# Performance work log

Hardware: AMD Instinct MI355X
Metric: run time of the kernel (lower is better)

The kernel has to match this reference:

```python
import jax, jax.numpy as jnp
import numpy as np

B, S = 2, 2048
IN, CD = 512, 128
HID, HEADS, DH = 1024, 8, 128
FFN, LAT, L = 4096, 256, 2


def _ln(x, s, b, eps=1e-5):
    m = x.mean(-1, keepdims=True)
    v = x.var(-1, keepdims=True)
    return (x - m) / jnp.sqrt(v + eps) * s + b


def _decay_mask():
    # D[h, n, m] = gamma_h^(n-m) for n >= m else 0; gamma_h = 1 - 2^(-5-h)
    n = jnp.arange(S)
    d = (n[:, None] - n[None, :]).astype(jnp.float32)
    mask = d >= 0
    expo = jnp.where(mask, d, 0.0)
    gammas = 1.0 - 2.0 ** (-5.0 - jnp.arange(HEADS, dtype=jnp.float32))
    return (gammas[:, None, None] ** expo[None]) * mask[None]


def setup_inputs() -> dict:
    key = jax.random.key(0)
    ks = jax.random.split(key, 20)
    f32 = jnp.float32
    def nrm(k, shape, s=0.02):
        return jax.random.normal(k, shape, f32) * s
    return {
        "x": jax.random.normal(ks[0], (B, S, IN), f32),
        "c": jax.random.normal(ks[1], (B, S, CD), f32),
        "W_in": nrm(ks[2], (IN + CD, HID)), "b_in": jnp.zeros((HID,), f32),
        "ln1_s": jnp.ones((L, HID), f32), "ln1_b": jnp.zeros((L, HID), f32),
        "Wq": nrm(ks[3], (L, HID, HID)), "Wk": nrm(ks[4], (L, HID, HID)),
        "Wv": nrm(ks[5], (L, HID, HID)), "Wg": nrm(ks[6], (L, HID, HID)),
        "Wo": nrm(ks[7], (L, HID, HID)),
        "gn_s": jnp.ones((L, HID), f32), "gn_b": jnp.zeros((L, HID), f32),
        "ln2_s": jnp.ones((L, HID), f32), "ln2_b": jnp.zeros((L, HID), f32),
        "W1": nrm(ks[8], (L, HID, FFN)), "b1": jnp.zeros((L, FFN), f32),
        "W2": nrm(ks[9], (L, FFN, HID)), "b2": jnp.zeros((L, HID), f32),
        "lnf_s": jnp.ones((HID,), f32), "lnf_b": jnp.zeros((HID,), f32),
        "W_mu": nrm(ks[10], (HID, LAT)), "b_mu": jnp.zeros((LAT,), f32),
        "W_lv": nrm(ks[11], (HID, LAT)), "b_lv": jnp.zeros((LAT,), f32),
    }


def reference(x, c, W_in, b_in, ln1_s, ln1_b, Wq, Wk, Wv, Wg, Wo, gn_s, gn_b,
              ln2_s, ln2_b, W1, b1, W2, b2, lnf_s, lnf_b, W_mu, b_mu, W_lv, b_lv):
    D = _decay_mask()                        # [H, S, S]
    h = jnp.concatenate([x, c], -1) @ W_in + b_in  # [B, S, HID]
    scale = 1.0 / np.sqrt(DH).astype(np.float32)
    for l in range(L):
        # --- multi-scale retention (parallel form) ---
        xn = _ln(h, ln1_s[l], ln1_b[l])
        q = (xn @ Wq[l]).reshape(B, S, HEADS, DH)
        k = (xn @ Wk[l]).reshape(B, S, HEADS, DH)
        v = (xn @ Wv[l]).reshape(B, S, HEADS, DH)
        scores = jnp.einsum('bnhd,bmhd->bhnm', q, k) * scale
        scores = scores * D[None]            # causal decay weighting
        o = jnp.einsum('bhnm,bmhd->bnhd', scores, v)
        # per-head group norm
        mu_ = o.mean(-1, keepdims=True)
        var_ = o.var(-1, keepdims=True)
        o = (o - mu_) / jnp.sqrt(var_ + 1e-5)
        o = o * gn_s[l].reshape(HEADS, DH) + gn_b[l].reshape(HEADS, DH)
        o = o.reshape(B, S, HID)
        g = jax.nn.silu(xn @ Wg[l])
        h = h + (g * o) @ Wo[l]
        # --- FFN ---
        xn2 = _ln(h, ln2_s[l], ln2_b[l])
        h = h + jax.nn.gelu(xn2 @ W1[l] + b1[l]) @ W2[l] + b2[l]
    h = _ln(h, lnf_s, lnf_b)
    mu = h @ W_mu + b_mu
    raw_logvar = h @ W_lv + b_lv
    std = jax.nn.softplus(0.5 * raw_logvar) + 0.001
    return mu, std
```

## Files before the change

kernel.cpp:

```cpp
#include <hip/hip_runtime.h>
#include <cmath>

typedef __bf16 bf16_t;
typedef __bf16 bf16x8 __attribute__((ext_vector_type(8)));
typedef float f32x4 __attribute__((ext_vector_type(4)));
typedef unsigned int u32x4 __attribute__((ext_vector_type(4)));

namespace {

constexpr int kS = 2048;
constexpr int kTok = 4096;
constexpr int kHid = 1024;
constexpr int kDh = 128;
constexpr float kScale = 0.08838834764831843f;

enum {
  EPI_BF16 = 0,
  EPI_BIAS_F32 = 2,
  EPI_RESID_F32 = 3,
  EPI_BIAS_GELU_BF16 = 4,
  EPI_MULV = 7,
  EPI_PART = 8,
};

__device__ __forceinline__ void gload16(const void* g, void* l) {
  __builtin_amdgcn_global_load_lds(
      (const __attribute__((address_space(1))) void*)g,
      (__attribute__((address_space(3))) void*)l, 16, 0, 0);
}

__device__ __forceinline__ f32x4 mfma16(bf16x8 a, bf16x8 b, f32x4 c) {
  return __builtin_amdgcn_mfma_f32_16x16x32_bf16(a, b, c, 0, 0, 0);
}

__device__ __forceinline__ unsigned xcd_swz(unsigned bid, unsigned nwg) {
  if ((nwg & 7u) != 0u) return bid;
  return (bid & 7u) * (nwg >> 3) + (bid >> 3);
}

__global__ __launch_bounds__(256) void build_a0_kernel(
    const float* __restrict__ x, const float* __restrict__ c,
    bf16_t* __restrict__ a0)
{
  int i = blockIdx.x * 256 + threadIdx.x;
  if (i >= kTok * 640) return;
  int t = i / 640;
  int col = i - t * 640;
  float v = (col < 512) ? x[(size_t)t * 512 + col]
                        : c[(size_t)t * 128 + (col - 512)];
  a0[i] = (bf16_t)v;
}

__global__ __launch_bounds__(256) void transpose_cast_kernel(
    const float* __restrict__ src, bf16_t* __restrict__ dst, int K, int N)
{
  __shared__ float tile[32][33];
  int n0 = blockIdx.x * 32, k0 = blockIdx.y * 32;
  int tx = threadIdx.x, ty = threadIdx.y;
#pragma unroll
  for (int ii = 0; ii < 4; ++ii) {
    int r = ty + ii * 8;
    tile[r][tx] = src[(size_t)(k0 + r) * N + (n0 + tx)];
  }
  __syncthreads();
#pragma unroll
  for (int ii = 0; ii < 4; ++ii) {
    int r = ty + ii * 8;
    dst[(size_t)(n0 + r) * K + (k0 + tx)] = (bf16_t)tile[tx][r];
  }
}

__global__ __launch_bounds__(256) void head_transpose_kernel(
    const bf16_t* __restrict__ in, int ld, bf16_t* __restrict__ out)
{
  __shared__ bf16_t tile[32][33];
  int s0 = blockIdx.x * 32;
  int d0 = blockIdx.y * 32;
  int bh = blockIdx.z;
  int b = bh >> 3, h = bh & 7;
  int tx = threadIdx.x & 31, ty = threadIdx.x >> 5;
#pragma unroll
  for (int ii = 0; ii < 4; ++ii) {
    int r = ty + ii * 8;
    tile[r][tx] = in[(size_t)(b * kS + s0 + r) * ld + h * kDh + d0 + tx];
  }
  __syncthreads();
#pragma unroll
  for (int ii = 0; ii < 4; ++ii) {
    int r = ty + ii * 8;
    out[((size_t)bh * kDh + d0 + r) * kS + s0 + tx] = tile[tx][r];
  }
}

__global__ __launch_bounds__(256) void ln_kernel(
    const float* __restrict__ H, const float* __restrict__ s,
    const float* __restrict__ b, bf16_t* __restrict__ out)
{
  const int t = blockIdx.x;
  const int tid = threadIdx.x;
  const float* row = H + (size_t)t * kHid;
  f32x4 x = *(const f32x4*)(row + tid * 4);
  float sum = x[0] + x[1] + x[2] + x[3];
  float ssq = x[0]*x[0] + x[1]*x[1] + x[2]*x[2] + x[3]*x[3];
#pragma unroll
  for (int m = 32; m >= 1; m >>= 1) {
    sum += __shfl_xor(sum, m, 64);
    ssq += __shfl_xor(ssq, m, 64);
  }
  __shared__ float red[8];
  int wave = tid >> 6;
  if ((tid & 63) == 0) { red[wave] = sum; red[4 + wave] = ssq; }
  __syncthreads();
  sum = red[0] + red[1] + red[2] + red[3];
  ssq = red[4] + red[5] + red[6] + red[7];
  float mean = sum * (1.0f / kHid);
  float var = ssq * (1.0f / kHid) - mean * mean;
  float rstd = rsqrtf(var + 1e-5f);
  bf16_t* orow = out + (size_t)t * kHid;
#pragma unroll
  for (int j = 0; j < 4; ++j) {
    int col = tid * 4 + j;
    orow[col] = (bf16_t)((x[j] - mean) * rstd * s[col] + b[col]);
  }
}

__global__ __launch_bounds__(256) void gn_gate_kernel(
    const float* __restrict__ o, const float* __restrict__ gns,
    const float* __restrict__ gnb, bf16_t* __restrict__ g, int ldg)
{
  int idx = blockIdx.x * 4 + (threadIdx.x >> 6);
  int lane = threadIdx.x & 63;
  size_t off = (size_t)idx * kDh;
  float v0 = o[off + lane * 2];
  float v1 = o[off + lane * 2 + 1];
  float sum = v0 + v1, ssq = v0 * v0 + v1 * v1;
#pragma unroll
  for (int m = 32; m >= 1; m >>= 1) {
    sum += __shfl_xor(sum, m, 64);
    ssq += __shfl_xor(ssq, m, 64);
  }
  float mean = sum * (1.0f / kDh);
  float var = ssq * (1.0f / kDh) - mean * mean;
  float rstd = rsqrtf(var + 1e-5f);
  int t = idx >> 3, h = idx & 7;
  int c0 = h * kDh + lane * 2;
  float s0 = gns[c0], s1 = gns[c0 + 1], b0 = gnb[c0], b1 = gnb[c0 + 1];
  size_t goff = (size_t)t * ldg + h * kDh + lane * 2;
  float g0 = (float)g[goff], g1 = (float)g[goff + 1];
  g0 = g0 / (1.0f + __expf(-g0));
  g1 = g1 / (1.0f + __expf(-g1));
  g[goff]     = (bf16_t)(((v0 - mean) * rstd * s0 + b0) * g0);
  g[goff + 1] = (bf16_t)(((v1 - mean) * rstd * s1 + b1) * g1);
}

template <int TM, int EPI>
__global__ __launch_bounds__(256) void gemm_kernel(
    const bf16_t* __restrict__ A, int lda, const bf16_t* __restrict__ Bt, int ldb,
    void* __restrict__ Cv, int ldc, const float* __restrict__ bias,
    const float* __restrict__ bias2, const float* __restrict__ resid,
    int M, int N, int kSpan)
{
  constexpr int MR = TM / 32;
  constexpr int ASEG = TM / 8;
  constexpr int TOT = ASEG + 16;
  constexpr int PER_WAVE = TOT / 4;
  __shared__ bf16_t As[2][TM * 64];
  __shared__ bf16_t Bs[2][128 * 64];
  const int tid = threadIdx.x;
  const int lane = tid & 63;
  const int wave = tid >> 6;
  const int wr = (wave >> 1) * (MR * 16);
  const int wc = (wave & 1) * 64;
  const unsigned nwg = gridDim.x * gridDim.y;
  const unsigned bid = xcd_swz(blockIdx.y * gridDim.x + blockIdx.x, nwg);
  const int bm = (bid % gridDim.x) * TM;
  const int bn = (bid / gridDim.x) * 128;
  const int kb = blockIdx.z * kSpan;
  const int r_ld = lane >> 3;
  const int cg = ((lane & 7) ^ r_ld) * 8;

  f32x4 acc[MR][4] = {};

  auto stage = [&](int bufi, int t) {
    int k0 = kb + t * 64;
#pragma unroll
    for (int i = 0; i < PER_WAVE; ++i) {
      int seg = wave * PER_WAVE + i;
      if (seg < ASEG) {
        int r = seg * 8 + r_ld;
        gload16(&A[(size_t)(bm + r) * lda + k0 + cg], &As[bufi][seg * 512]);
      } else {
        int s2 = seg - ASEG;
        int r = s2 * 8 + r_ld;
        gload16(&Bt[(size_t)(bn + r) * ldb + k0 + cg], &Bs[bufi][s2 * 512]);
      }
    }
  };
  auto compute = [&](int bufi) {
#pragma unroll
    for (int kk = 0; kk < 64; kk += 32) {
      const int cg0 = (kk >> 3) + (lane >> 4);
      bf16x8 af[MR], bfr[4];
#pragma unroll
      for (int m = 0; m < MR; ++m) {
        int row = wr + m * 16 + (lane & 15);
        af[m] = *(const bf16x8*)&As[bufi][row * 64 + ((cg0 ^ (row & 7)) << 3)];
      }
#pragma unroll
      for (int n = 0; n < 4; ++n) {
        int row = wc + n * 16 + (lane & 15);
        bfr[n] = *(const bf16x8*)&Bs[bufi][row * 64 + ((cg0 ^ (row & 7)) << 3)];
      }
#pragma unroll
      for (int m = 0; m < MR; ++m)
#pragma unroll
        for (int n = 0; n < 4; ++n)
          acc[m][n] = mfma16(af[m], bfr[n], acc[m][n]);
    }
  };

  const int nt = kSpan >> 6;
  stage(0, 0);
  stage(1, 1);
  for (int t = 0; t < nt; ++t) {
    if (t + 1 < nt) {
      if constexpr (PER_WAVE == 8) asm volatile("s_waitcnt vmcnt(8)" ::: "memory");
      else                         asm volatile("s_waitcnt vmcnt(6)" ::: "memory");
    } else {
      asm volatile("s_waitcnt vmcnt(0)" ::: "memory");
    }
    __builtin_amdgcn_s_barrier();
    compute(t & 1);
    __builtin_amdgcn_s_barrier();
    if (t + 2 < nt) stage(t & 1, t + 2);
  }

  const int cr = (lane >> 4) * 4;
  const int cc = lane & 15;
#pragma unroll
  for (int m = 0; m < MR; ++m) {
#pragma unroll
    for (int n = 0; n < 4; ++n) {
#pragma unroll
      for (int j = 0; j < 4; ++j) {
        int gr = bm + wr + m * 16 + cr + j;
        int gc = bn + wc + n * 16 + cc;
        size_t off = (size_t)gr * ldc + gc;
        float v = acc[m][n][j];
        if constexpr (EPI == EPI_BF16) {
          ((bf16_t*)Cv)[off] = (bf16_t)v;
        } else if constexpr (EPI == EPI_BIAS_F32) {
          ((float*)Cv)[off] = v + bias[gc];
        } else if constexpr (EPI == EPI_RESID_F32) {
          ((float*)Cv)[off] = v + resid[off];
        } else if constexpr (EPI == EPI_BIAS_GELU_BF16) {
          v += bias[gc];
          float u3 = v + 0.044715f * v * v * v;
          float th = tanhf(0.7978845608028654f * u3);
          ((bf16_t*)Cv)[off] = (bf16_t)(0.5f * v * (1.0f + th));
        } else if constexpr (EPI == EPI_PART) {
          ((float*)Cv)[(size_t)blockIdx.z * M * N + off] = v;
        } else if constexpr (EPI == EPI_MULV) {
          if (gc < 256) {
            ((float*)Cv)[(size_t)gr * 256 + gc] = v + bias[gc];
          } else {
            float r2 = 0.5f * (v + bias2[gc - 256]);
            float sp = (r2 > 20.0f) ? r2 : log1pf(__expf(r2));
            ((float*)Cv)[(size_t)4096 * 256 + (size_t)gr * 256 + (gc - 256)] = sp + 0.001f;
          }
        }
      }
    }
  }
}

template <int EPI>
__global__ __launch_bounds__(512, 2) void gemm256_kernel(
    const bf16_t* __restrict__ A, int lda, const bf16_t* __restrict__ Bt, int ldb,
    void* __restrict__ Cv, int ldc, const float* __restrict__ bias,
    int M, int N, int kSpan)
{
  __shared__ bf16_t As[2][256 * 64];
  __shared__ bf16_t Bs[2][256 * 64];
  const int tid = threadIdx.x;
  const int lane = tid & 63;
  const int wave = tid >> 6;
  const int wm = wave >> 2;
  const int wn = wave & 3;
  const unsigned nwg = gridDim.x * gridDim.y;
  const unsigned bid = xcd_swz(blockIdx.y * gridDim.x + blockIdx.x, nwg);
  const int bm = (bid % gridDim.x) * 256;
  const int bn = (bid / gridDim.x) * 256;
  const int kb = blockIdx.z * kSpan;
  const int r_ld = lane >> 3;
  const int cgs = ((lane & 7) ^ r_ld) * 8;
  const int rl15 = lane & 15, rl7 = lane & 7, rhi = lane >> 4;

  f32x4 acc[8][4] = {};

  const bf16_t* pA0a; const bf16_t* pA0b;
  const bf16_t* pA1a; const bf16_t* pA1b;
  const bf16_t* pB0a; const bf16_t* pB0b;
  const bf16_t* pB1a; const bf16_t* pB1b;
  int sg0a, sg0b, sg1a, sg1b;
  {
    int s0a = 0 * 16 + wave * 2 + 0, s0b = 0 * 16 + wave * 2 + 1;
    int s1a = 1 * 16 + wave * 2 + 0, s1b = 1 * 16 + wave * 2 + 1;
    sg0a = s0a * 512; sg0b = s0b * 512; sg1a = s1a * 512; sg1b = s1b * 512;
    pA0a = A + (size_t)(bm + s0a * 8 + r_ld) * lda + kb + cgs;
    pA0b = A + (size_t)(bm + s0b * 8 + r_ld) * lda + kb + cgs;
    pA1a = A + (size_t)(bm + s1a * 8 + r_ld) * lda + kb + cgs;
    pA1b = A + (size_t)(bm + s1b * 8 + r_ld) * lda + kb + cgs;
    pB0a = Bt + (size_t)(bn + s0a * 8 + r_ld) * ldb + kb + cgs;
    pB0b = Bt + (size_t)(bn + s0b * 8 + r_ld) * ldb + kb + cgs;
    pB1a = Bt + (size_t)(bn + s1a * 8 + r_ld) * ldb + kb + cgs;
    pB1b = Bt + (size_t)(bn + s1b * 8 + r_ld) * ldb + kb + cgs;
  }
  auto stageA0 = [&](int bufi) {
    gload16(pA0a, &As[bufi][sg0a]); gload16(pA0b, &As[bufi][sg0b]);
  };
  auto stageA1 = [&](int bufi) {
    gload16(pA1a, &As[bufi][sg1a]); gload16(pA1b, &As[bufi][sg1b]);
  };
  auto stageB0 = [&](int bufi) {
    gload16(pB0a, &Bs[bufi][sg0a]); gload16(pB0b, &Bs[bufi][sg0b]);
  };
  auto stageB1 = [&](int bufi) {
    gload16(pB1a, &Bs[bufi][sg1a]); gload16(pB1b, &Bs[bufi][sg1b]);
  };
  auto advance = [&]() {
    pA0a += 64; pA0b += 64; pA1a += 64; pA1b += 64;
    pB0a += 64; pB0b += 64; pB1a += 64; pB1b += 64;
  };
  auto lda_frag = [&](int bufi, int mf, int kk) -> bf16x8 {
    int row = wm * 128 + mf * 16 + rl15;
    int cg0 = (kk >> 3) + rhi;
    return *(const bf16x8*)&As[bufi][row * 64 + ((cg0 ^ rl7) << 3)];
  };
  auto ldb_frag = [&](int bufi, int nf, int kk) -> bf16x8 {
    int row = wn * 64 + nf * 16 + rl15;
    int cg0 = (kk >> 3) + rhi;
    return *(const bf16x8*)&Bs[bufi][row * 64 + ((cg0 ^ rl7) << 3)];
  };

  const int nt = kSpan >> 6;
  stageA0(0); stageB0(0); stageB1(0); stageA1(0);
  advance();

  bf16x8 bk0[4], bk1[4], af[4];
  int cb = 0;

  for (int t = 0; t < nt - 1; ++t) {
    const int nb = cb ^ 1;
    asm volatile("s_waitcnt vmcnt(4)" ::: "memory");
    __builtin_amdgcn_s_barrier();
#pragma unroll
    for (int nf = 0; nf < 4; ++nf) bk0[nf] = ldb_frag(cb, nf, 0);
#pragma unroll
    for (int mf = 0; mf < 4; ++mf) af[mf] = lda_frag(cb, mf, 0);
    stageA0(nb); stageB0(nb);
    asm volatile("s_waitcnt lgkmcnt(0)" ::: "memory");
    __builtin_amdgcn_sched_barrier(0);
    __builtin_amdgcn_s_setprio(1);
#pragma unroll
    for (int mf = 0; mf < 4; ++mf)
#pragma unroll
      for (int nf = 0; nf < 4; ++nf)
        acc[mf][nf] = mfma16(af[mf], bk0[nf], acc[mf][nf]);
    __builtin_amdgcn_s_setprio(0);
    asm volatile("s_waitcnt vmcnt(6)" ::: "memory");
    __builtin_amdgcn_s_barrier();
#pragma unroll
    for (int nf = 0; nf < 4; ++nf) bk1[nf] = ldb_frag(cb, nf, 32);
#pragma unroll
    for (int mf = 0; mf < 4; ++mf) af[mf] = lda_frag(cb, mf, 32);
    stageB1(nb);
    asm volatile("s_waitcnt lgkmcnt(0)" ::: "memory");
    __builtin_amdgcn_sched_barrier(0);
    __builtin_amdgcn_s_setprio(1);
#pragma unroll
    for (int mf = 0; mf < 4; ++mf)
#pragma unroll
      for (int nf = 0; nf < 4; ++nf)
        acc[mf][nf] = mfma16(af[mf], bk1[nf], acc[mf][nf]);
    __builtin_amdgcn_s_setprio(0);
    asm volatile("s_waitcnt vmcnt(6)" ::: "memory");
    __builtin_amdgcn_s_barrier();
#pragma unroll
    for (int mf = 0; mf < 4; ++mf) af[mf] = lda_frag(cb, 4 + mf, 0);
    stageA1(nb);
    asm volatile("s_waitcnt lgkmcnt(0)" ::: "memory");
    __builtin_amdgcn_sched_barrier(0);
    __builtin_amdgcn_s_setprio(1);
#pragma unroll
    for (int mf = 0; mf < 4; ++mf)
#pragma unroll
      for (int nf = 0; nf < 4; ++nf)
        acc[4 + mf][nf] = mfma16(af[mf], bk0[nf], acc[4 + mf][nf]);
    __builtin_amdgcn_s_setprio(0);
#pragma unroll
    for (int mf = 0; mf < 4; ++mf) af[mf] = lda_frag(cb, 4 + mf, 32);
    asm volatile("s_waitcnt lgkmcnt(0)" ::: "memory");
    __builtin_amdgcn_sched_barrier(0);
    __builtin_amdgcn_s_setprio(1);
#pragma unroll
    for (int mf = 0; mf < 4; ++mf)
#pragma unroll
      for (int nf = 0; nf < 4; ++nf)
        acc[4 + mf][nf] = mfma16(af[mf], bk1[nf], acc[4 + mf][nf]);
    __builtin_amdgcn_s_setprio(0);
    advance();
    cb ^= 1;
  }

  {
    asm volatile("s_waitcnt vmcnt(0)" ::: "memory");
    __builtin_amdgcn_s_barrier();
#pragma unroll
    for (int nf = 0; nf < 4; ++nf) bk0[nf] = ldb_frag(cb, nf, 0);
#pragma unroll
    for (int nf = 0; nf < 4; ++nf) bk1[nf] = ldb_frag(cb, nf, 32);
#pragma unroll
    for (int half = 0; half < 2; ++half) {
#pragma unroll
      for (int mf = 0; mf < 4; ++mf) af[mf] = lda_frag(cb, half * 4 + mf, 0);
      asm volatile("s_waitcnt lgkmcnt(0)" ::: "memory");
      __builtin_amdgcn_sched_barrier(0);
#pragma unroll
      for (int mf = 0; mf < 4; ++mf)
#pragma unroll
        for (int nf = 0; nf < 4; ++nf)
          acc[half * 4 + mf][nf] = mfma16(af[mf], bk0[nf], acc[half * 4 + mf][nf]);
#pragma unroll
      for (int mf = 0; mf < 4; ++mf) af[mf] = lda_frag(cb, half * 4 + mf, 32);
      asm volatile("s_waitcnt lgkmcnt(0)" ::: "memory");
      __builtin_amdgcn_sched_barrier(0);
#pragma unroll
      for (int mf = 0; mf < 4; ++mf)
#pragma unroll
        for (int nf = 0; nf < 4; ++nf)
          acc[half * 4 + mf][nf] = mfma16(af[mf], bk1[nf], acc[half * 4 + mf][nf]);
    }
  }

  const int cr = rhi * 4;
  const int cc = rl15;
#pragma unroll
  for (int mf = 0; mf < 8; ++mf) {
#pragma unroll
    for (int nf = 0; nf < 4; ++nf) {
#pragma unroll
      for (int j = 0; j < 4; ++j) {
        int gr = bm + wm * 128 + mf * 16 + cr + j;
        int gc = bn + wn * 64 + nf * 16 + cc;
        size_t off = (size_t)gr * ldc + gc;
        float v = acc[mf][nf][j];
        if constexpr (EPI == EPI_BF16) {
          ((bf16_t*)Cv)[off] = (bf16_t)v;
        } else if constexpr (EPI == EPI_BIAS_GELU_BF16) {
          v += bias[gc];
          float u3 = v + 0.044715f * v * v * v;
          float th = tanhf(0.7978845608028654f * u3);
          ((bf16_t*)Cv)[off] = (bf16_t)(0.5f * v * (1.0f + th));
        } else if constexpr (EPI == EPI_PART) {
          ((float*)Cv)[(size_t)blockIdx.z * M * N + off] = v;
        }
      }
    }
  }
}

__global__ __launch_bounds__(256) void ffn2_reduce_kernel(
    const float* __restrict__ P, const float* __restrict__ b2,
    float* __restrict__ H)
{
  int i = blockIdx.x * 256 + threadIdx.x;
  size_t e = (size_t)i * 4;
  int col = (int)(e & 1023);
  f32x4 a = *(const f32x4*)&P[e];
  f32x4 b = *(const f32x4*)&P[(size_t)4096 * 1024 + e];
  f32x4 h = *(const f32x4*)&H[e];
  f32x4 bb = *(const f32x4*)&b2[col];
  f32x4 r = { h[0] + a[0] + b[0] + bb[0], h[1] + a[1] + b[1] + bb[1],
              h[2] + a[2] + b[2] + bb[2], h[3] + a[3] + b[3] + bb[3] };
  *(f32x4*)&H[e] = r;
}

__global__ __launch_bounds__(256) void chunk_state_kernel(
    const bf16_t* __restrict__ KT, const bf16_t* __restrict__ VT,
    bf16_t* __restrict__ U)
{
  __shared__ bf16_t Ka[128][72];
  __shared__ bf16_t Va[128][72];
  const int tid = threadIdx.x, lane = tid & 63, wave = tid >> 6;
  const int t = blockIdx.x, bh = blockIdx.y, h = bh & 7;
  const float lg2g = log2f(1.0f - exp2f(-5.0f - (float)h));
#pragma unroll
  for (int it = 0; it < 4; ++it) {
    int u = tid + it * 256;
    int r = u >> 3, cg = (u & 7) * 8;
    size_t g = ((size_t)bh * kDh + r) * kS + t * 64 + cg;
    *(u32x4*)&Va[r][cg] = *(const u32x4*)&VT[g];
    bf16x8 kv = *(const bf16x8*)&KT[g];
    bf16x8 ks;
#pragma unroll
    for (int j = 0; j < 8; ++j)
      ks[j] = (bf16_t)((float)kv[j] * exp2f((float)(63 - (cg + j)) * lg2g));
    *(bf16x8*)&Ka[r][cg] = ks;
  }
  __syncthreads();
  f32x4 acc[2][8] = {};
#pragma unroll
  for (int kk = 0; kk < 64; kk += 32) {
    bf16x8 af[2], bfr[8];
#pragma unroll
    for (int m = 0; m < 2; ++m)
      af[m] = *(const bf16x8*)&Va[wave * 32 + m * 16 + (lane & 15)][kk + (lane >> 4) * 8];
#pragma unroll
    for (int n = 0; n < 8; ++n)
      bfr[n] = *(const bf16x8*)&Ka[n * 16 + (lane & 15)][kk + (lane >> 4) * 8];
#pragma unroll
    for (int m = 0; m < 2; ++m)
#pragma unroll
      for (int n = 0; n < 8; ++n)
        acc[m][n] = mfma16(af[m], bfr[n], acc[m][n]);
  }
  size_t base = ((size_t)bh * 32 + t) * 16384;
#pragma unroll
  for (int m = 0; m < 2; ++m)
#pragma unroll
    for (int n = 0; n < 8; ++n)
#pragma unroll
      for (int j = 0; j < 4; ++j) {
        int dv = wave * 32 + m * 16 + (lane >> 4) * 4 + j;
        int dk = n * 16 + (lane & 15);
        U[base + dv * 128 + dk] = (bf16_t)acc[m][n][j];
      }
}

__global__ __launch_bounds__(256) void chunk_scan_kernel(
    const bf16_t* __restrict__ U, bf16_t* __restrict__ S)
{
  int e = blockIdx.x * 256 + threadIdx.x;
  int bh = blockIdx.y, h = bh & 7;
  float d64 = exp2f(64.0f * log2f(1.0f - exp2f(-5.0f - (float)h)));
  float s = 0.0f;
  size_t base = (size_t)bh * 32 * 16384 + e;
  for (int t = 0; t < 32; ++t) {
    size_t idx = base + (size_t)t * 16384;
    float u = (float)U[idx];
    S[idx] = (bf16_t)s;
    s = d64 * s + u;
  }
}

__global__ __launch_bounds__(256) void chunk_out_kernel(
    const bf16_t* __restrict__ QB, const bf16_t* __restrict__ KB, int ldq,
    const bf16_t* __restrict__ VT, const bf16_t* __restrict__ S,
    float* __restrict__ OF)
{
  __shared__ bf16_t Qs[64][136];
  __shared__ bf16_t Ks[64][136];
  __shared__ bf16_t Vs[128][72];
  __shared__ bf16_t Ps[64][72];
  const int tid = threadIdx.x, lane = tid & 63, wave = tid >> 6;
  const int t = blockIdx.x, bh = blockIdx.y;
  const int b = bh >> 3, h = bh & 7;
  const float lg2g = log2f(1.0f - exp2f(-5.0f - (float)h));

#pragma unroll
  for (int it = 0; it < 4; ++it) {
    int u = tid + it * 256;
    int r = u >> 4, cg = (u & 15) * 8;
    size_t g = ((size_t)b * kS + t * 64 + r) * ldq + h * kDh + cg;
    *(u32x4*)&Qs[r][cg] = *(const u32x4*)&QB[g];
    *(u32x4*)&Ks[r][cg] = *(const u32x4*)&KB[g];
    int rv = u >> 3, cv = (u & 7) * 8;
    *(u32x4*)&Vs[rv][cv] = *(const u32x4*)&VT[((size_t)bh * kDh + rv) * kS + t * 64 + cv];
  }
  __syncthreads();

  f32x4 sf[4] = {};
#pragma unroll
  for (int kk = 0; kk < 128; kk += 32) {
    bf16x8 aq = *(const bf16x8*)&Qs[wave * 16 + (lane & 15)][kk + (lane >> 4) * 8];
#pragma unroll
    for (int c2 = 0; c2 < 4; ++c2) {
      bf16x8 bk = *(const bf16x8*)&Ks[c2 * 16 + (lane & 15)][kk + (lane >> 4) * 8];
      sf[c2] = mfma16(aq, bk, sf[c2]);
    }
  }
#pragma unroll
  for (int c2 = 0; c2 < 4; ++c2)
#pragma unroll
    for (int j = 0; j < 4; ++j) {
      int nl = wave * 16 + (lane >> 4) * 4 + j;
      int ml = c2 * 16 + (lane & 15);
      int d = nl - ml;
      float w = (d >= 0) ? kScale * exp2f((float)d * lg2g) : 0.0f;
      Ps[nl][ml] = (bf16_t)(sf[c2][j] * w);
    }
  __syncthreads();

  f32x4 oa[8] = {}, oi[8] = {};
#pragma unroll
  for (int ks = 0; ks < 64; ks += 32) {
    bf16x8 ap = *(const bf16x8*)&Ps[wave * 16 + (lane & 15)][ks + (lane >> 4) * 8];
#pragma unroll
    for (int dt = 0; dt < 8; ++dt) {
      bf16x8 bv = *(const bf16x8*)&Vs[dt * 16 + (lane & 15)][ks + (lane >> 4) * 8];
      oa[dt] = mfma16(ap, bv, oa[dt]);
    }
  }
  size_t sbase = ((size_t)bh * 32 + t) * 16384;
#pragma unroll
  for (int kk = 0; kk < 128; kk += 32) {
    bf16x8 aq = *(const bf16x8*)&Qs[wave * 16 + (lane & 15)][kk + (lane >> 4) * 8];
#pragma unroll
    for (int dt = 0; dt < 8; ++dt) {
      bf16x8 bs = *(const bf16x8*)&S[sbase + (size_t)(dt * 16 + (lane & 15)) * 128 + kk + (lane >> 4) * 8];
      oi[dt] = mfma16(aq, bs, oi[dt]);
    }
  }
#pragma unroll
  for (int dt = 0; dt < 8; ++dt)
#pragma unroll
    for (int j = 0; j < 4; ++j) {
      int nl = wave * 16 + (lane >> 4) * 4 + j;
      float gf = kScale * exp2f((float)(nl + 1) * lg2g);
      OF[((size_t)b * kS + t * 64 + nl) * kHid + h * kDh + dt * 16 + (lane & 15)] =
          oa[dt][j] + gf * oi[dt][j];
    }
}

template <int TM>
void launch_gemm(int epi, const bf16_t* A, int lda, const bf16_t* Bt, int ldb,
                 void* C, int ldc, const float* bias, const float* bias2,
                 const float* resid, int M, int N, int K, int ksplit, hipStream_t st)
{
  dim3 g(M / TM, N / 128, ksplit), b(256);
  int kSpan = K / ksplit;
  switch (epi) {
    case EPI_BF16:           gemm_kernel<TM, EPI_BF16><<<g, b, 0, st>>>(A, lda, Bt, ldb, C, ldc, bias, bias2, resid, M, N, kSpan); break;
    case EPI_BIAS_F32:       gemm_kernel<TM, EPI_BIAS_F32><<<g, b, 0, st>>>(A, lda, Bt, ldb, C, ldc, bias, bias2, resid, M, N, kSpan); break;
    case EPI_RESID_F32:      gemm_kernel<TM, EPI_RESID_F32><<<g, b, 0, st>>>(A, lda, Bt, ldb, C, ldc, bias, bias2, resid, M, N, kSpan); break;
    case EPI_BIAS_GELU_BF16: gemm_kernel<TM, EPI_BIAS_GELU_BF16><<<g, b, 0, st>>>(A, lda, Bt, ldb, C, ldc, bias, bias2, resid, M, N, kSpan); break;
    case EPI_PART:           gemm_kernel<TM, EPI_PART><<<g, b, 0, st>>>(A, lda, Bt, ldb, C, ldc, bias, bias2, resid, M, N, kSpan); break;
    case EPI_MULV:           gemm_kernel<TM, EPI_MULV><<<g, b, 0, st>>>(A, lda, Bt, ldb, C, ldc, bias, bias2, resid, M, N, kSpan); break;
  }
}

void launch_transpose(const float* src, bf16_t* dst, int K, int N, hipStream_t st) {
  transpose_cast_kernel<<<dim3(N / 32, K / 32), dim3(32, 8), 0, st>>>(src, dst, K, N);
}

}

extern "C" void kernel_launch(void* const* d_in, const int* in_sizes, int n_in,
                              void* d_out, int out_size, void* d_ws, size_t ws_size,
                              hipStream_t stream) {
  const float* x     = (const float*)d_in[0];
  const float* c     = (const float*)d_in[1];
  const float* W_in  = (const float*)d_in[2];
  const float* b_in  = (const float*)d_in[3];
  const float* ln1_s = (const float*)d_in[4];
  const float* ln1_b = (const float*)d_in[5];
  const float* Wq    = (const float*)d_in[6];
  const float* Wk    = (const float*)d_in[7];
  const float* Wv    = (const float*)d_in[8];
  const float* Wg    = (const float*)d_in[9];
  const float* Wo    = (const float*)d_in[10];
  const float* gn_s  = (const float*)d_in[11];
  const float* gn_b  = (const float*)d_in[12];
  const float* ln2_s = (const float*)d_in[13];
  const float* ln2_b = (const float*)d_in[14];
  const float* W1    = (const float*)d_in[15];
  const float* b1    = (const float*)d_in[16];
  const float* W2    = (const float*)d_in[17];
  const float* b2    = (const float*)d_in[18];
  const float* lnf_s = (const float*)d_in[19];
  const float* lnf_b = (const float*)d_in[20];
  const float* W_mu  = (const float*)d_in[21];
  const float* b_mu  = (const float*)d_in[22];
  const float* W_lv  = (const float*)d_in[23];
  const float* b_lv  = (const float*)d_in[24];

  char* p = (char*)d_ws;
  bf16_t* WT   = (bf16_t*)p; p += (size_t)4096 * 1024 * 2;
  bf16_t* A0   = (bf16_t*)p; p += (size_t)4096 * 640 * 2;
  float*  H    = (float*) p; p += (size_t)4096 * 1024 * 4;
  bf16_t* XN   = (bf16_t*)p; p += (size_t)4096 * 1024 * 2;
  bf16_t* QKVG = (bf16_t*)p; p += (size_t)4096 * 4096 * 2;
  bf16_t* Sb   = (bf16_t*)p; p += (size_t)16 * 32 * 16384 * 2;
  float*  OF   = (float*) p; p += (size_t)4096 * 1024 * 4;
  bf16_t* F1 = QKVG;
  bf16_t* KT = WT;
  bf16_t* VT = XN;
  bf16_t* Ub = (bf16_t*)OF;
  float*  PART = (float*)Sb;

  build_a0_kernel<<<dim3((kTok * 640 + 255) / 256), dim3(256), 0, stream>>>(x, c, A0);
  launch_transpose(W_in, WT, 640, 1024, stream);
  launch_gemm<64>(EPI_BIAS_F32, A0, 640, WT, 640, H, 1024, b_in, nullptr, nullptr,
                  4096, 1024, 640, 1, stream);

  for (int l = 0; l < 2; ++l) {
    const size_t wsq = (size_t)l * 1024 * 1024;
    ln_kernel<<<dim3(4096), dim3(256), 0, stream>>>(H, ln1_s + l * 1024, ln1_b + l * 1024, XN);

    launch_transpose(Wq + wsq, WT,                      1024, 1024, stream);
    launch_transpose(Wk + wsq, WT + ((size_t)1 << 20),  1024, 1024, stream);
    launch_transpose(Wv + wsq, WT + ((size_t)2 << 20),  1024, 1024, stream);
    launch_transpose(Wg + wsq, WT + ((size_t)3 << 20),  1024, 1024, stream);
    gemm256_kernel<EPI_BF16><<<dim3(16, 16, 1), dim3(512), 0, stream>>>(
        XN, 1024, WT, 1024, QKVG, 4096, nullptr, 4096, 4096, 1024);

    head_transpose_kernel<<<dim3(64, 4, 16), dim3(256), 0, stream>>>(QKVG + 1024, 4096, KT);
    head_transpose_kernel<<<dim3(64, 4, 16), dim3(256), 0, stream>>>(QKVG + 2048, 4096, VT);
    chunk_state_kernel<<<dim3(32, 16), dim3(256), 0, stream>>>(KT, VT, Ub);
    chunk_scan_kernel<<<dim3(64, 16), dim3(256), 0, stream>>>(Ub, (bf16_t*)Sb);
    chunk_out_kernel<<<dim3(32, 16), dim3(256), 0, stream>>>(QKVG, QKVG + 1024, 4096, VT, (bf16_t*)Sb, OF);

    gn_gate_kernel<<<dim3(8192), dim3(256), 0, stream>>>(OF, gn_s + l * 1024, gn_b + l * 1024,
                                                         QKVG + 3072, 4096);

    launch_transpose(Wo + wsq, WT, 1024, 1024, stream);
    launch_gemm<64>(EPI_RESID_F32, QKVG + 3072, 4096, WT, 1024, H, 1024, nullptr, nullptr, H,
                    4096, 1024, 1024, 1, stream);

    ln_kernel<<<dim3(4096), dim3(256), 0, stream>>>(H, ln2_s + l * 1024, ln2_b + l * 1024, XN);
    launch_transpose(W1 + (size_t)l * 1024 * 4096, WT, 1024, 4096, stream);
    gemm256_kernel<EPI_BIAS_GELU_BF16><<<dim3(16, 16, 1), dim3(512), 0, stream>>>(
        XN, 1024, WT, 1024, F1, 4096, b1 + l * 4096, 4096, 4096, 1024);
    launch_transpose(W2 + (size_t)l * 4096 * 1024, WT, 4096, 1024, stream);
    launch_gemm<128>(EPI_PART, F1, 4096, WT, 4096, PART, 1024, nullptr, nullptr, nullptr,
                     4096, 1024, 4096, 2, stream);
    ffn2_reduce_kernel<<<dim3(4096), dim3(256), 0, stream>>>(PART, b2 + l * 1024, H);
  }

  ln_kernel<<<dim3(4096), dim3(256), 0, stream>>>(H, lnf_s, lnf_b, XN);
  launch_transpose(W_mu, WT, 1024, 256, stream);
  launch_transpose(W_lv, WT + (size_t)256 * 1024, 1024, 256, stream);
  launch_gemm<64>(EPI_MULV, XN, 1024, WT, 1024, d_out, 512, b_mu, b_lv, nullptr,
                  4096, 512, 1024, 1, stream);
}
```

Before: 553.3 us.

## Fuse group-norm and SiLU gate into chunk_out; batch weight and head transposes

```diff
diff --git a/kernel.cpp b/kernel.cpp
--- a/kernel.cpp
+++ b/kernel.cpp
@@ -70,13 +70,41 @@
   }
 }
 
-__global__ __launch_bounds__(256) void head_transpose_kernel(
-    const bf16_t* __restrict__ in, int ld, bf16_t* __restrict__ out)
+__global__ __launch_bounds__(256) void transpose_cast4_kernel(
+    const float* __restrict__ w0, const float* __restrict__ w1,
+    const float* __restrict__ w2, const float* __restrict__ w3,
+    bf16_t* __restrict__ dst, int K, int N)
+{
+  __shared__ float tile[32][33];
+  int z = blockIdx.z;
+  const float* src = (z == 0) ? w0 : (z == 1) ? w1 : (z == 2) ? w2 : w3;
+  bf16_t* d = dst + (size_t)z * N * K;
+  int n0 = blockIdx.x * 32, k0 = blockIdx.y * 32;
+  int tx = threadIdx.x & 31, ty = threadIdx.x >> 5;
+#pragma unroll
+  for (int ii = 0; ii < 4; ++ii) {
+    int r = ty + ii * 8;
+    tile[r][tx] = src[(size_t)(k0 + r) * N + (n0 + tx)];
+  }
+  __syncthreads();
+#pragma unroll
+  for (int ii = 0; ii < 4; ++ii) {
+    int r = ty + ii * 8;
+    d[(size_t)(n0 + r) * K + (k0 + tx)] = (bf16_t)tile[tx][r];
+  }
+}
+
+__global__ __launch_bounds__(256) void head_transpose2_kernel(
+    const bf16_t* __restrict__ inK, const bf16_t* __restrict__ inV, int ld,
+    bf16_t* __restrict__ outK, bf16_t* __restrict__ outV)
 {
   __shared__ bf16_t tile[32][33];
+  int zz = blockIdx.z;
+  int bh = zz & 15;
+  const bf16_t* in = (zz < 16) ? inK : inV;
+  bf16_t* out = (zz < 16) ? outK : outV;
   int s0 = blockIdx.x * 32;
   int d0 = blockIdx.y * 32;
-  int bh = blockIdx.z;
   int b = bh >> 3, h = bh & 7;
   int tx = threadIdx.x & 31, ty = threadIdx.x >> 5;
 #pragma unroll
@@ -122,35 +150,6 @@
     int col = tid * 4 + j;
     orow[col] = (bf16_t)((x[j] - mean) * rstd * s[col] + b[col]);
   }
-}
-
-__global__ __launch_bounds__(256) void gn_gate_kernel(
-    const float* __restrict__ o, const float* __restrict__ gns,
-    const float* __restrict__ gnb, bf16_t* __restrict__ g, int ldg)
-{
-  int idx = blockIdx.x * 4 + (threadIdx.x >> 6);
-  int lane = threadIdx.x & 63;
-  size_t off = (size_t)idx * kDh;
-  float v0 = o[off + lane * 2];
-  float v1 = o[off + lane * 2 + 1];
-  float sum = v0 + v1, ssq = v0 * v0 + v1 * v1;
-#pragma unroll
-  for (int m = 32; m >= 1; m >>= 1) {
-    sum += __shfl_xor(sum, m, 64);
-    ssq += __shfl_xor(ssq, m, 64);
-  }
-  float mean = sum * (1.0f / kDh);
-  float var = ssq * (1.0f / kDh) - mean * mean;
-  float rstd = rsqrtf(var + 1e-5f);
-  int t = idx >> 3, h = idx & 7;
-  int c0 = h * kDh + lane * 2;
-  float s0 = gns[c0], s1 = gns[c0 + 1], b0 = gnb[c0], b1 = gnb[c0 + 1];
-  size_t goff = (size_t)t * ldg + h * kDh + lane * 2;
-  float g0 = (float)g[goff], g1 = (float)g[goff + 1];
-  g0 = g0 / (1.0f + __expf(-g0));
-  g1 = g1 / (1.0f + __expf(-g1));
-  g[goff]     = (bf16_t)(((v0 - mean) * rstd * s0 + b0) * g0);
-  g[goff + 1] = (bf16_t)(((v1 - mean) * rstd * s1 + b1) * g1);
 }
 
 template <int TM, int EPI>
@@ -557,7 +556,8 @@
 __global__ __launch_bounds__(256) void chunk_out_kernel(
     const bf16_t* __restrict__ QB, const bf16_t* __restrict__ KB, int ldq,
     const bf16_t* __restrict__ VT, const bf16_t* __restrict__ S,
-    float* __restrict__ OF)
+    const float* __restrict__ gns, const float* __restrict__ gnb,
+    bf16_t* __restrict__ G)
 {
   __shared__ bf16_t Qs[64][136];
   __shared__ bf16_t Ks[64][136];
@@ -622,15 +622,46 @@
       oi[dt] = mfma16(aq, bs, oi[dt]);
     }
   }
+
+  float gf[4];
+#pragma unroll
+  for (int j = 0; j < 4; ++j) {
+    int nl = wave * 16 + (lane >> 4) * 4 + j;
+    gf[j] = kScale * exp2f((float)(nl + 1) * lg2g);
+  }
 #pragma unroll
   for (int dt = 0; dt < 8; ++dt)
 #pragma unroll
-    for (int j = 0; j < 4; ++j) {
-      int nl = wave * 16 + (lane >> 4) * 4 + j;
-      float gf = kScale * exp2f((float)(nl + 1) * lg2g);
-      OF[((size_t)b * kS + t * 64 + nl) * kHid + h * kDh + dt * 16 + (lane & 15)] =
-          oa[dt][j] + gf * oi[dt][j];
-    }
+    for (int j = 0; j < 4; ++j)
+      oa[dt][j] = oa[dt][j] + gf[j] * oi[dt][j];
+
+  float sc[8], bb[8];
+#pragma unroll
+  for (int dt = 0; dt < 8; ++dt) {
+    int col = h * kDh + dt * 16 + (lane & 15);
+    sc[dt] = gns[col]; bb[dt] = gnb[col];
+  }
+#pragma unroll
+  for (int j = 0; j < 4; ++j) {
+    float s = 0.f, q = 0.f;
+#pragma unroll
+    for (int dt = 0; dt < 8; ++dt) { float v = oa[dt][j]; s += v; q += v * v; }
+    s += __shfl_xor(s, 1, 64); q += __shfl_xor(q, 1, 64);
+    s += __shfl_xor(s, 2, 64); q += __shfl_xor(q, 2, 64);
+    s += __shfl_xor(s, 4, 64); q += __shfl_xor(q, 4, 64);
+    s += __shfl_xor(s, 8, 64); q += __shfl_xor(q, 8, 64);
+    float mean = s * (1.0f / kDh);
+    float var = q * (1.0f / kDh) - mean * mean;
+    float rstd = rsqrtf(var + 1e-5f);
+    int nl = wave * 16 + (lane >> 4) * 4 + j;
+    size_t rowoff = ((size_t)b * kS + t * 64 + nl) * 4096 + h * kDh + (lane & 15);
+#pragma unroll
+    for (int dt = 0; dt < 8; ++dt) {
+      float gv = (float)G[rowoff + dt * 16];
+      gv = gv / (1.0f + __expf(-gv));
+      G[rowoff + dt * 16] = (bf16_t)(((oa[dt][j] - mean) * rstd * sc[dt] + bb[dt]) * gv);
+    }
+  }
 }
 
 template <int TM>
@@ -708,21 +739,18 @@
     const size_t wsq = (size_t)l * 1024 * 1024;
     ln_kernel<<<dim3(4096), dim3(256), 0, stream>>>(H, ln1_s + l * 1024, ln1_b + l * 1024, XN);
 
-    launch_transpose(Wq + wsq, WT,                      1024, 1024, stream);
-    launch_transpose(Wk + wsq, WT + ((size_t)1 << 20),  1024, 1024, stream);
-    launch_transpose(Wv + wsq, WT + ((size_t)2 << 20),  1024, 1024, stream);
-    launch_transpose(Wg + wsq, WT + ((size_t)3 << 20),  1024, 1024, stream);
+    transpose_cast4_kernel<<<dim3(32, 32, 4), dim3(256), 0, stream>>>(
+        Wq + wsq, Wk + wsq, Wv + wsq, Wg + wsq, WT, 1024, 1024);
     gemm256_kernel<EPI_BF16><<<dim3(16, 16, 1), dim3(512), 0, stream>>>(
         XN, 1024, WT, 1024, QKVG, 4096, nullptr, 4096, 4096, 1024);
 
-    head_transpose_kernel<<<dim3(64, 4, 16), dim3(256), 0, stream>>>(QKVG + 1024, 4096, KT);
-    head_transpose_kernel<<<dim3(64, 4, 16), dim3(256), 0, stream>>>(QKVG + 2048, 4096, VT);
+    head_transpose2_kernel<<<dim3(64, 4, 32), dim3(256), 0, stream>>>(
+        QKVG + 1024, QKVG + 2048, 4096, KT, VT);
     chunk_state_kernel<<<dim3(32, 16), dim3(256), 0, stream>>>(KT, VT, Ub);
     chunk_scan_kernel<<<dim3(64, 16), dim3(256), 0, stream>>>(Ub, (bf16_t*)Sb);
-    chunk_out_kernel<<<dim3(32, 16), dim3(256), 0, stream>>>(QKVG, QKVG + 1024, 4096, VT, (bf16_t*)Sb, OF);
-
-    gn_gate_kernel<<<dim3(8192), dim3(256), 0, stream>>>(OF, gn_s + l * 1024, gn_b + l * 1024,
-                                                         QKVG + 3072, 4096);
+    chunk_out_kernel<<<dim3(32, 16), dim3(256), 0, stream>>>(
+        QKVG, QKVG + 1024, 4096, VT, (bf16_t*)Sb,
+        gn_s + l * 1024, gn_b + l * 1024, QKVG + 3072);
 
     launch_transpose(Wo + wsq, WT, 1024, 1024, stream);
     launch_gemm<64>(EPI_RESID_F32, QKVG + 3072, 4096, WT, 1024, H, 1024, nullptr, nullptr, H,
@@ -739,8 +767,8 @@
   }
 
   ln_kernel<<<dim3(4096), dim3(256), 0, stream>>>(H, lnf_s, lnf_b, XN);
-  launch_transpose(W_mu, WT, 1024, 256, stream);
-  launch_transpose(W_lv, WT + (size_t)256 * 1024, 1024, 256, stream);
+  transpose_cast4_kernel<<<dim3(8, 32, 2), dim3(256), 0, stream>>>(
+      W_mu, W_lv, W_mu, W_lv, WT, 1024, 256);
   launch_gemm<64>(EPI_MULV, XN, 1024, WT, 1024, d_out, 512, b_mu, b_lv, nullptr,
                   4096, 512, 1024, 1, stream);
 }
```

New measurement: 524.7 us. 5.2% less time.
